# Optimization experiments

Measured on AMD Instinct MI355X. Metric: run time of the kernel, lower is better.

The kernel has to match this reference:

```python
import jax, jax.numpy as jnp
import numpy as np

B, H, S, D = 2, 16, 2048, 64

def setup_inputs() -> dict:
    key = jax.random.key(0)
    kq, kk, kv = jax.random.split(key, 3)
    q = jax.random.normal(kq, (B, H, S, D), dtype=jnp.float32)
    k = jax.random.normal(kk, (B, H, S, D), dtype=jnp.float32)
    v = jax.random.normal(kv, (B, H, S, D), dtype=jnp.float32)
    # causal mask: True where position j > i (future tokens are masked)
    mask = jnp.triu(jnp.ones((S, S), dtype=bool), k=1)[None, None, :, :]
    return {"q": q, "k": k, "v": v, "mask": mask}

def reference(q, k, v, mask) -> jnp.ndarray:
    # scaled dot-product attention with additive -1e4 mask bias
    scale = 1.0 / jnp.sqrt(jnp.asarray(q.shape[-1], q.dtype))
    scores = jnp.einsum('bhqd,bhkd->bhqk', q, k) * scale  # [B,H,S,S]
    scores = scores + mask.astype(scores.dtype) * jnp.asarray(-10000.0, scores.dtype)
    probs = jax.nn.softmax(scores, axis=-1)
    # dropout is identity in eval mode
    return jnp.einsum('bhqk,bhkd->bhqd', probs, v)
```

## Files before the change

### kernel.cpp

```cpp
#include <hip/hip_runtime.h>

typedef __bf16 bf16_t;
typedef bf16_t bf16x8 __attribute__((ext_vector_type(8)));
typedef bf16_t bf16x4 __attribute__((ext_vector_type(4)));
typedef float  floatx4 __attribute__((ext_vector_type(4)));

constexpr int Sq = 2048, Dq = 64;
constexpr int BQ = 64, BK = 64;
constexpr int NQT = Sq / BQ;
constexpr int STR = 72;
constexpr float SCALE_LOG2E = 0.125f * 1.44269504088896340736f;

__global__ __launch_bounds__(256, 2) void flash_attn_kernel(
    const float* __restrict__ Q, const float* __restrict__ K,
    const float* __restrict__ V, float* __restrict__ O)
{
    __shared__ bf16_t QPs[BQ][STR];
    __shared__ bf16_t Ks[BK][STR];
    __shared__ bf16_t VTs[Dq][STR];

    const int tid  = threadIdx.x;
    const int wave = tid >> 6;
    const int lane = tid & 63;
    const int quad = lane >> 4;
    const int l16  = lane & 15;

    const int id = blockIdx.x;
    const int bh = (id & 7) + ((id >> 7) << 3);
    const int pr = (id >> 3) & 15;
    const long base = (long)bh * Sq * Dq;

    const int r0 = tid >> 4;
    const int c4 = (tid & 15) * 4;
    const int h  = lane >> 3;
    const int jw = wave * 16;

    for (int half = 0; half < 2; ++half) {
        const int qt = half ? (NQT - 1 - pr) : pr;

        __syncthreads();
        #pragma unroll
        for (int p = 0; p < 4; ++p) {
            const int row = p * 16 + r0;
            const float4 qv = *(const float4*)&Q[base + (long)(qt * BQ + row) * Dq + c4];
            bf16x4 w;
            w[0] = (bf16_t)(qv.x * SCALE_LOG2E); w[1] = (bf16_t)(qv.y * SCALE_LOG2E);
            w[2] = (bf16_t)(qv.z * SCALE_LOG2E); w[3] = (bf16_t)(qv.w * SCALE_LOG2E);
            *(bf16x4*)&QPs[row][c4] = w;
        }
        __syncthreads();

        bf16x8 aq0, aq1;
        {
            const int qrow = wave * 16 + l16;
            aq0 = *(const bf16x8*)&QPs[qrow][quad * 8];
            aq1 = *(const bf16x8*)&QPs[qrow][32 + quad * 8];
        }

        float l_lane = 0.f;
        floatx4 o_acc[4];
        #pragma unroll
        for (int i = 0; i < 4; ++i) o_acc[i] = floatx4{0.f, 0.f, 0.f, 0.f};

        float4 kf[4];
        float  vf[4][4];
        #pragma unroll
        for (int p = 0; p < 4; ++p) {
            kf[p] = *(const float4*)&K[base + (long)(p * 16 + r0) * Dq + c4];
            const int j0 = jw + 4 * ((p + h) & 3);
            #pragma unroll
            for (int r = 0; r < 4; ++r)
                vf[p][r] = V[base + (long)(j0 + r) * Dq + lane];
        }

        for (int kt = 0; kt <= qt; ++kt) {
            __syncthreads();

            #pragma unroll
            for (int p = 0; p < 4; ++p) {
                bf16x4 w;
                w[0] = (bf16_t)kf[p].x; w[1] = (bf16_t)kf[p].y;
                w[2] = (bf16_t)kf[p].z; w[3] = (bf16_t)kf[p].w;
                *(bf16x4*)&Ks[p * 16 + r0][c4] = w;
                bf16x4 vw;
                vw[0] = (bf16_t)vf[p][0]; vw[1] = (bf16_t)vf[p][1];
                vw[2] = (bf16_t)vf[p][2]; vw[3] = (bf16_t)vf[p][3];
                *(bf16x4*)&VTs[lane][jw + 4 * ((p + h) & 3)] = vw;
            }
            __syncthreads();

            {
                const int kn = (kt < qt) ? (kt + 1) : qt;
                const long kb = base + (long)kn * BK * Dq;
                #pragma unroll
                for (int p = 0; p < 4; ++p) {
                    kf[p] = *(const float4*)&K[kb + (long)(p * 16 + r0) * Dq + c4];
                    const int j0 = jw + 4 * ((p + h) & 3);
                    #pragma unroll
                    for (int r = 0; r < 4; ++r)
                        vf[p][r] = V[kb + (long)(j0 + r) * Dq + lane];
                }
            }

            floatx4 acc[4];
            #pragma unroll
            for (int t = 0; t < 4; ++t) {
                acc[t] = floatx4{0.f, 0.f, 0.f, 0.f};
                const int krow = t * 16 + l16;
                bf16x8 ak0 = *(const bf16x8*)&Ks[krow][quad * 8];
                bf16x8 ak1 = *(const bf16x8*)&Ks[krow][32 + quad * 8];
                acc[t] = __builtin_amdgcn_mfma_f32_16x16x32_bf16(ak0, aq0, acc[t], 0, 0, 0);
                acc[t] = __builtin_amdgcn_mfma_f32_16x16x32_bf16(ak1, aq1, acc[t], 0, 0, 0);
            }

            if (kt == qt) {
                const int qr = wave * 16 + l16;
                #pragma unroll
                for (int t = 0; t < 4; ++t) {
                    #pragma unroll
                    for (int i = 0; i < 4; ++i) {
                        if (t * 16 + quad * 4 + i > qr) acc[t][i] = -1e30f;
                    }
                }
            }

            float l_add = 0.f;
            #pragma unroll
            for (int t = 0; t < 4; ++t) {
                #pragma unroll
                for (int i = 0; i < 4; ++i) {
                    acc[t][i] = __builtin_amdgcn_exp2f(acc[t][i]);
                    l_add += acc[t][i];
                }
            }
            l_lane += l_add;

            #pragma unroll
            for (int t = 0; t < 4; ++t) {
                bf16x4 pk;
                pk[0] = (bf16_t)acc[t][0]; pk[1] = (bf16_t)acc[t][1];
                pk[2] = (bf16_t)acc[t][2]; pk[3] = (bf16_t)acc[t][3];
                *(bf16x4*)&QPs[wave * 16 + l16][t * 16 + quad * 4] = pk;
            }

            bf16x8 ap0 = *(const bf16x8*)&QPs[wave * 16 + l16][quad * 8];
            bf16x8 ap1 = *(const bf16x8*)&QPs[wave * 16 + l16][32 + quad * 8];
            #pragma unroll
            for (int dt = 0; dt < 4; ++dt) {
                const int dcol = dt * 16 + l16;
                bf16x8 bv0 = *(const bf16x8*)&VTs[dcol][quad * 8];
                bf16x8 bv1 = *(const bf16x8*)&VTs[dcol][32 + quad * 8];
                o_acc[dt] = __builtin_amdgcn_mfma_f32_16x16x32_bf16(ap0, bv0, o_acc[dt], 0, 0, 0);
                o_acc[dt] = __builtin_amdgcn_mfma_f32_16x16x32_bf16(ap1, bv1, o_acc[dt], 0, 0, 0);
            }
        }

        float lsum = l_lane;
        lsum += __shfl_xor(lsum, 16);
        lsum += __shfl_xor(lsum, 32);
        #pragma unroll
        for (int i = 0; i < 4; ++i) {
            const float inv_l = 1.f / __shfl(lsum, quad * 4 + i, 16);
            const long row = (long)qt * BQ + wave * 16 + quad * 4 + i;
            #pragma unroll
            for (int dt = 0; dt < 4; ++dt) {
                O[base + row * Dq + dt * 16 + l16] = o_acc[dt][i] * inv_l;
            }
        }
    }
}

extern "C" void kernel_launch(void* const* d_in, const int* in_sizes, int n_in,
                              void* d_out, int out_size, void* d_ws, size_t ws_size,
                              hipStream_t stream)
{
    const float* q = (const float*)d_in[0];
    const float* k = (const float*)d_in[1];
    const float* v = (const float*)d_in[2];
    float* out = (float*)d_out;
    flash_attn_kernel<<<dim3(512, 1, 1), dim3(256, 1, 1), 0, stream>>>(q, k, v, out);
}
```

Measured before the change: 128.2 us.

## Rewrite flash attention with 128-row Q tiles, split-KV wave groups, 32x32 MFMA

Reworks the kernel so each 512-thread block owns a 128-row query tile. Two 256-thread groups process alternating KV tiles, with double-buffered XOR-swizzled LDS and partial outputs merged through shared memory at the end. Q is kept in registers and the score/PV products use 32x32x16 MFMAs. P is repacked with permlane32_swap instead of a round trip through LDS, and s_setprio hints are added. This is meant to raise per-block reuse and MFMA efficiency and cut LDS traffic, at the cost of halving the block count and adding an epilogue reduction.

New measurement: 143.8 us. 1.12x slower.

```diff
diff --git a/kernel.cpp b/kernel.cpp
--- a/kernel.cpp
+++ b/kernel.cpp
@@ -1,170 +1,227 @@
 #include <hip/hip_runtime.h>
 
 typedef __bf16 bf16_t;
+typedef bf16_t bf16x2 __attribute__((ext_vector_type(2)));
+typedef bf16_t bf16x4 __attribute__((ext_vector_type(4)));
 typedef bf16_t bf16x8 __attribute__((ext_vector_type(8)));
-typedef bf16_t bf16x4 __attribute__((ext_vector_type(4)));
-typedef float  floatx4 __attribute__((ext_vector_type(4)));
+typedef float  floatx16 __attribute__((ext_vector_type(16)));
+typedef unsigned int uintx4 __attribute__((ext_vector_type(4)));
 
 constexpr int Sq = 2048, Dq = 64;
-constexpr int BQ = 64, BK = 64;
+constexpr int BQ = 128;
+constexpr int KVB = 64;
 constexpr int NQT = Sq / BQ;
-constexpr int STR = 72;
 constexpr float SCALE_LOG2E = 0.125f * 1.44269504088896340736f;
 
-__global__ __launch_bounds__(256, 2) void flash_attn_kernel(
+struct LoopS { bf16_t K[2][2][KVB * Dq]; bf16_t V[2][2][Dq * KVB]; };
+struct EpiS  { float Op[BQ][Dq]; float den[BQ]; };
+union  SmemU { LoopS l; EpiS e; };
+
+static __device__ __forceinline__ bf16x8 cvt8(const float4& a, const float4& b) {
+    bf16x8 w;
+    w[0] = (bf16_t)a.x; w[1] = (bf16_t)a.y; w[2] = (bf16_t)a.z; w[3] = (bf16_t)a.w;
+    w[4] = (bf16_t)b.x; w[5] = (bf16_t)b.y; w[6] = (bf16_t)b.z; w[7] = (bf16_t)b.w;
+    return w;
+}
+static __device__ __forceinline__ bf16x8 cvt8s(const float4& a, const float4& b) {
+    bf16x8 w;
+    w[0] = (bf16_t)(a.x * SCALE_LOG2E); w[1] = (bf16_t)(a.y * SCALE_LOG2E);
+    w[2] = (bf16_t)(a.z * SCALE_LOG2E); w[3] = (bf16_t)(a.w * SCALE_LOG2E);
+    w[4] = (bf16_t)(b.x * SCALE_LOG2E); w[5] = (bf16_t)(b.y * SCALE_LOG2E);
+    w[6] = (bf16_t)(b.z * SCALE_LOG2E); w[7] = (bf16_t)(b.w * SCALE_LOG2E);
+    return w;
+}
+static __device__ __forceinline__ unsigned int pkbf(float lo, float hi) {
+    bf16x2 t; t[0] = (bf16_t)lo; t[1] = (bf16_t)hi;
+    return __builtin_bit_cast(unsigned int, t);
+}
+
+#define SUM16(p) (((((p)[0]+(p)[1])+((p)[2]+(p)[3]))+(((p)[4]+(p)[5])+((p)[6]+(p)[7]))) \
+                + ((((p)[8]+(p)[9])+((p)[10]+(p)[11]))+(((p)[12]+(p)[13])+((p)[14]+(p)[15]))))
+
+#define LOADKV(kt) do {                                                        \
+    const long kb_ = base + (long)(kt) * KVB * Dq;                             \
+    const float* ks_ = &K[kb_ + (long)krow_st * Dq + kd0];                     \
+    kr0 = *(const float4*)&ks_[0];  kr1 = *(const float4*)&ks_[4];             \
+    kr2 = *(const float4*)&ks_[8];  kr3 = *(const float4*)&ks_[12];            \
+    _Pragma("unroll")                                                          \
+    for (int p_ = 0; p_ < 4; ++p_) {                                           \
+        const int j0_ = vjw + 4 * ((p_ + vh) & 3);                             \
+        _Pragma("unroll")                                                      \
+        for (int r_ = 0; r_ < 4; ++r_)                                         \
+            vraw[p_][r_] = V[kb_ + (long)(j0_ + r_) * Dq + vd];                \
+    } } while (0)
+
+#define WRITEKV(kdst, vdst) do {                                               \
+    char* kc_ = (char*)(kdst) + krow_st * 128;                                 \
+    const int ksw_ = (krow_st & 7) << 4;                                       \
+    *(bf16x8*)(kc_ + ((2 * kd0) ^ ksw_))      = cvt8(kr0, kr1);                \
+    *(bf16x8*)(kc_ + ((2 * kd0 + 16) ^ ksw_)) = cvt8(kr2, kr3);                \
+    char* vc_ = (char*)(vdst) + vd * 128;                                      \
+    const int vsw_ = (vd & 7) << 4;                                            \
+    _Pragma("unroll")                                                          \
+    for (int p_ = 0; p_ < 4; ++p_) {                                           \
+        const int j0_ = vjw + 4 * ((p_ + vh) & 3);                             \
+        bf16x4 vw_;                                                            \
+        vw_[0] = (bf16_t)vraw[p_][0]; vw_[1] = (bf16_t)vraw[p_][1];            \
+        vw_[2] = (bf16_t)vraw[p_][2]; vw_[3] = (bf16_t)vraw[p_][3];            \
+        *(bf16x4*)(vc_ + ((2 * j0_) ^ vsw_)) = vw_;                            \
+    } } while (0)
+
+__global__ __launch_bounds__(512, 2) void flash_attn_kernel(
     const float* __restrict__ Q, const float* __restrict__ K,
     const float* __restrict__ V, float* __restrict__ O)
 {
-    __shared__ bf16_t QPs[BQ][STR];
-    __shared__ bf16_t Ks[BK][STR];
-    __shared__ bf16_t VTs[Dq][STR];
+    __shared__ SmemU sm;
 
     const int tid  = threadIdx.x;
-    const int wave = tid >> 6;
-    const int lane = tid & 63;
-    const int quad = lane >> 4;
-    const int l16  = lane & 15;
+    const int grp  = tid >> 8;
+    const int gtid = tid & 255;
+    const int wave = gtid >> 6;
+    const int lane = gtid & 63;
+    const int hi   = lane >> 5;
+    const int l31  = lane & 31;
 
     const int id = blockIdx.x;
-    const int bh = (id & 7) + ((id >> 7) << 3);
-    const int pr = (id >> 3) & 15;
+    const int bh = (id & 7) + ((id >> 6) << 3);
+    const int pr = (id >> 3) & 7;
     const long base = (long)bh * Sq * Dq;
 
-    const int r0 = tid >> 4;
-    const int c4 = (tid & 15) * 4;
-    const int h  = lane >> 3;
-    const int jw = wave * 16;
+    const int krow_st = gtid >> 2;
+    const int kd0     = 16 * (gtid & 3);
+    const int vd      = gtid & 63;
+    const int vjw     = 16 * (gtid >> 6);
+    const int vh      = (gtid & 63) >> 3;
+
+    bf16_t* const Kb0 = &sm.l.K[grp][0][0];
+    bf16_t* const Kb1 = &sm.l.K[grp][1][0];
+    bf16_t* const Vb0 = &sm.l.V[grp][0][0];
+    bf16_t* const Vb1 = &sm.l.V[grp][1][0];
+    const int lsw = (l31 & 7) << 4;
 
     for (int half = 0; half < 2; ++half) {
         const int qt = half ? (NQT - 1 - pr) : pr;
+        const long qb = base + (long)qt * BQ * Dq;
+        const int qrow = 32 * wave + l31;
+        const int niter = qt + 1;
+
+        bf16x8 qf[4];
+        #pragma unroll
+        for (int ss = 0; ss < 4; ++ss) {
+            const float* qp = &Q[qb + (long)qrow * Dq + 16 * ss + 8 * hi];
+            qf[ss] = cvt8s(*(const float4*)&qp[0], *(const float4*)&qp[4]);
+        }
+
+        float4 kr0, kr1, kr2, kr3;
+        float  vraw[4][4];
 
         __syncthreads();
-        #pragma unroll
-        for (int p = 0; p < 4; ++p) {
-            const int row = p * 16 + r0;
-            const float4 qv = *(const float4*)&Q[base + (long)(qt * BQ + row) * Dq + c4];
-            bf16x4 w;
-            w[0] = (bf16_t)(qv.x * SCALE_LOG2E); w[1] = (bf16_t)(qv.y * SCALE_LOG2E);
-            w[2] = (bf16_t)(qv.z * SCALE_LOG2E); w[3] = (bf16_t)(qv.w * SCALE_LOG2E);
-            *(bf16x4*)&QPs[row][c4] = w;
-        }
+        LOADKV(grp);
+        WRITEKV(Kb0, Vb0);
         __syncthreads();
 
-        bf16x8 aq0, aq1;
-        {
-            const int qrow = wave * 16 + l16;
-            aq0 = *(const bf16x8*)&QPs[qrow][quad * 8];
-            aq1 = *(const bf16x8*)&QPs[qrow][32 + quad * 8];
-        }
-
         float l_lane = 0.f;
-        floatx4 o_acc[4];
-        #pragma unroll
-        for (int i = 0; i < 4; ++i) o_acc[i] = floatx4{0.f, 0.f, 0.f, 0.f};
-
-        float4 kf[4];
-        float  vf[4][4];
-        #pragma unroll
-        for (int p = 0; p < 4; ++p) {
-            kf[p] = *(const float4*)&K[base + (long)(p * 16 + r0) * Dq + c4];
-            const int j0 = jw + 4 * ((p + h) & 3);
+        floatx16 oacc[2];
+        oacc[0] = (floatx16)0.f; oacc[1] = (floatx16)0.f;
+
+        for (int i = 0; i < niter; ++i) {
+            const int kt = 2 * i + grp;
+            const bool more = (i + 1 < niter);
+            if (more) LOADKV(kt + 2);
+
+            if (64 * kt <= BQ * qt + 32 * wave + 31) {
+                const bf16_t* kbase = (i & 1) ? Kb1 : Kb0;
+                const bf16_t* vbase = (i & 1) ? Vb1 : Vb0;
+
+                floatx16 s0 = (floatx16)0.f, s1 = (floatx16)0.f;
+                __builtin_amdgcn_s_setprio(1);
+                #pragma unroll
+                for (int ss = 0; ss < 4; ++ss) {
+                    const int cb = (32 * ss + 16 * hi) ^ lsw;
+                    bf16x8 k0 = *(const bf16x8*)((const char*)kbase + l31 * 128 + cb);
+                    bf16x8 k1 = *(const bf16x8*)((const char*)kbase + (32 + l31) * 128 + cb);
+                    s0 = __builtin_amdgcn_mfma_f32_32x32x16_bf16(k0, qf[ss], s0, 0, 0, 0);
+                    s1 = __builtin_amdgcn_mfma_f32_32x32x16_bf16(k1, qf[ss], s1, 0, 0, 0);
+                }
+                __builtin_amdgcn_s_setprio(0);
+
+                float p0[16], p1[16];
+                const bool diag = (kt >= 2 * qt);
+                const int kg0 = 64 * kt;
+                const int qg  = BQ * qt + qrow;
+                #pragma unroll
+                for (int r = 0; r < 16; ++r) {
+                    const int cr = (r & 3) + 8 * (r >> 2) + 4 * hi;
+                    float a = s0[r], b = s1[r];
+                    if (diag) {
+                        if (kg0 + cr > qg)      a = -1e30f;
+                        if (kg0 + 32 + cr > qg) b = -1e30f;
+                    }
+                    p0[r] = __builtin_amdgcn_exp2f(a);
+                    p1[r] = __builtin_amdgcn_exp2f(b);
+                }
+                l_lane += SUM16(p0) + SUM16(p1);
+
+                unsigned int w[4][4];
+                #pragma unroll
+                for (int s = 0; s < 4; ++s) {
+                    const float* pt = (s >> 1) ? p1 : p0;
+                    const int R = 8 * (s & 1);
+                    unsigned int c0 = pkbf(pt[R + 0], pt[R + 1]);
+                    unsigned int c1 = pkbf(pt[R + 2], pt[R + 3]);
+                    unsigned int d0 = pkbf(pt[R + 4], pt[R + 5]);
+                    unsigned int d1 = pkbf(pt[R + 6], pt[R + 7]);
+                    asm volatile("v_permlane32_swap_b32 %0, %1" : "+v"(c0), "+v"(d0));
+                    asm volatile("v_permlane32_swap_b32 %0, %1" : "+v"(c1), "+v"(d1));
+                    w[s][0] = c0; w[s][1] = c1; w[s][2] = d0; w[s][3] = d1;
+                }
+
+                __builtin_amdgcn_s_setprio(1);
+                #pragma unroll
+                for (int t2 = 0; t2 < 2; ++t2) {
+                    #pragma unroll
+                    for (int s = 0; s < 4; ++s) {
+                        uintx4 fw; fw[0] = w[s][0]; fw[1] = w[s][1];
+                        fw[2] = w[s][2]; fw[3] = w[s][3];
+                        const bf16x8 pa = __builtin_bit_cast(bf16x8, fw);
+                        const int cb = (32 * s + 16 * hi) ^ lsw;
+                        bf16x8 vf = *(const bf16x8*)((const char*)vbase + (32 * t2 + l31) * 128 + cb);
+                        oacc[t2] = __builtin_amdgcn_mfma_f32_32x32x16_bf16(pa, vf, oacc[t2], 0, 0, 0);
+                    }
+                }
+                __builtin_amdgcn_s_setprio(0);
+            }
+
+            if (more) WRITEKV((i & 1) ? Kb0 : Kb1, (i & 1) ? Vb0 : Vb1);
+            __syncthreads();
+        }
+
+        const float lden = l_lane + __shfl_xor(l_lane, 32);
+
+        if (grp == 1) {
             #pragma unroll
-            for (int r = 0; r < 4; ++r)
-                vf[p][r] = V[base + (long)(j0 + r) * Dq + lane];
-        }
-
-        for (int kt = 0; kt <= qt; ++kt) {
-            __syncthreads();
-
+            for (int t2 = 0; t2 < 2; ++t2)
+                #pragma unroll
+                for (int r = 0; r < 16; ++r) {
+                    const int cr = (r & 3) + 8 * (r >> 2) + 4 * hi;
+                    sm.e.Op[32 * wave + cr][32 * t2 + l31] = oacc[t2][r];
+                }
+            if (hi == 0) sm.e.den[32 * wave + l31] = lden;
+        }
+        __syncthreads();
+        if (grp == 0) {
             #pragma unroll
-            for (int p = 0; p < 4; ++p) {
-                bf16x4 w;
-                w[0] = (bf16_t)kf[p].x; w[1] = (bf16_t)kf[p].y;
-                w[2] = (bf16_t)kf[p].z; w[3] = (bf16_t)kf[p].w;
-                *(bf16x4*)&Ks[p * 16 + r0][c4] = w;
-                bf16x4 vw;
-                vw[0] = (bf16_t)vf[p][0]; vw[1] = (bf16_t)vf[p][1];
-                vw[2] = (bf16_t)vf[p][2]; vw[3] = (bf16_t)vf[p][3];
-                *(bf16x4*)&VTs[lane][jw + 4 * ((p + h) & 3)] = vw;
-            }
-            __syncthreads();
-
-            {
-                const int kn = (kt < qt) ? (kt + 1) : qt;
-                const long kb = base + (long)kn * BK * Dq;
-                #pragma unroll
-                for (int p = 0; p < 4; ++p) {
-                    kf[p] = *(const float4*)&K[kb + (long)(p * 16 + r0) * Dq + c4];
-                    const int j0 = jw + 4 * ((p + h) & 3);
-                    #pragma unroll
-                    for (int r = 0; r < 4; ++r)
-                        vf[p][r] = V[kb + (long)(j0 + r) * Dq + lane];
-                }
-            }
-
-            floatx4 acc[4];
-            #pragma unroll
-            for (int t = 0; t < 4; ++t) {
-                acc[t] = floatx4{0.f, 0.f, 0.f, 0.f};
-                const int krow = t * 16 + l16;
-                bf16x8 ak0 = *(const bf16x8*)&Ks[krow][quad * 8];
-                bf16x8 ak1 = *(const bf16x8*)&Ks[krow][32 + quad * 8];
-                acc[t] = __builtin_amdgcn_mfma_f32_16x16x32_bf16(ak0, aq0, acc[t], 0, 0, 0);
-                acc[t] = __builtin_amdgcn_mfma_f32_16x16x32_bf16(ak1, aq1, acc[t], 0, 0, 0);
-            }
-
-            if (kt == qt) {
-                const int qr = wave * 16 + l16;
-                #pragma unroll
-                for (int t = 0; t < 4; ++t) {
-                    #pragma unroll
-                    for (int i = 0; i < 4; ++i) {
-                        if (t * 16 + quad * 4 + i > qr) acc[t][i] = -1e30f;
-                    }
-                }
-            }
-
-            float l_add = 0.f;
-            #pragma unroll
-            for (int t = 0; t < 4; ++t) {
-                #pragma unroll
-                for (int i = 0; i < 4; ++i) {
-                    acc[t][i] = __builtin_amdgcn_exp2f(acc[t][i]);
-                    l_add += acc[t][i];
-                }
-            }
-            l_lane += l_add;
-
-            #pragma unroll
-            for (int t = 0; t < 4; ++t) {
-                bf16x4 pk;
-                pk[0] = (bf16_t)acc[t][0]; pk[1] = (bf16_t)acc[t][1];
-                pk[2] = (bf16_t)acc[t][2]; pk[3] = (bf16_t)acc[t][3];
-                *(bf16x4*)&QPs[wave * 16 + l16][t * 16 + quad * 4] = pk;
-            }
-
-            bf16x8 ap0 = *(const bf16x8*)&QPs[wave * 16 + l16][quad * 8];
-            bf16x8 ap1 = *(const bf16x8*)&QPs[wave * 16 + l16][32 + quad * 8];
-            #pragma unroll
-            for (int dt = 0; dt < 4; ++dt) {
-                const int dcol = dt * 16 + l16;
-                bf16x8 bv0 = *(const bf16x8*)&VTs[dcol][quad * 8];
-                bf16x8 bv1 = *(const bf16x8*)&VTs[dcol][32 + quad * 8];
-                o_acc[dt] = __builtin_amdgcn_mfma_f32_16x16x32_bf16(ap0, bv0, o_acc[dt], 0, 0, 0);
-                o_acc[dt] = __builtin_amdgcn_mfma_f32_16x16x32_bf16(ap1, bv1, o_acc[dt], 0, 0, 0);
-            }
-        }
-
-        float lsum = l_lane;
-        lsum += __shfl_xor(lsum, 16);
-        lsum += __shfl_xor(lsum, 32);
-        #pragma unroll
-        for (int i = 0; i < 4; ++i) {
-            const float inv_l = 1.f / __shfl(lsum, quad * 4 + i, 16);
-            const long row = (long)qt * BQ + wave * 16 + quad * 4 + i;
-            #pragma unroll
-            for (int dt = 0; dt < 4; ++dt) {
-                O[base + row * Dq + dt * 16 + l16] = o_acc[dt][i] * inv_l;
+            for (int r = 0; r < 16; ++r) {
+                const int cr = (r & 3) + 8 * (r >> 2) + 4 * hi;
+                const float dA = __shfl(lden, cr);
+                const float dB = sm.e.den[32 * wave + cr];
+                const float inv = 1.f / (dA + dB);
+                const long orow = qb + (long)(32 * wave + cr) * Dq;
+                #pragma unroll
+                for (int t2 = 0; t2 < 2; ++t2) {
+                    const float ov = oacc[t2][r] + sm.e.Op[32 * wave + cr][32 * t2 + l31];
+                    O[orow + 32 * t2 + l31] = ov * inv;
+                }
             }
         }
     }
@@ -178,5 +235,5 @@
     const float* k = (const float*)d_in[1];
     const float* v = (const float*)d_in[2];
     float* out = (float*)d_out;
-    flash_attn_kernel<<<dim3(512, 1, 1), dim3(256, 1, 1), 0, stream>>>(q, k, v, out);
-}
+    flash_attn_kernel<<<dim3(256, 1, 1), dim3(512, 1, 1), 0, stream>>>(q, k, v, out);
+}
```
